# Performance work log

Hardware: AMD Instinct MI355X
Metric: run time of the kernel (lower is better)

Reference implementation:

```python
import jax, jax.numpy as jnp
import numpy as np

CHAR_SIZE, WORD_SIZE = 200, 100000
EC, EW, HID = 128, 300, 512
H2 = HID // 2
NW, TC = 1024, 16
POS, NER = 48, 16


def lstm_layer(x, Wih, Whh, b, reverse=False):
    """PyTorch-gate-order LSTM. x: [T, ..., D] -> [T, ..., H]."""
    H = Whh.shape[1]
    init = (jnp.zeros(x.shape[1:-1] + (H,), x.dtype),) * 2
    def step(carry, xt):
        h, c = carry
        z = xt @ Wih.T + h @ Whh.T + b
        i, f, g, o = jnp.split(z, 4, axis=-1)
        c = jax.nn.sigmoid(f) * c + jax.nn.sigmoid(i) * jnp.tanh(g)
        h = jax.nn.sigmoid(o) * jnp.tanh(c)
        return (h, c), h
    _, hs = jax.lax.scan(step, init, x, reverse=reverse)
    return hs


def bilstm(x, pf, pb):
    hf = lstm_layer(x, *pf)
    hb = lstm_layer(x, *pb, reverse=True)
    return jnp.concatenate([hf, hb], axis=-1)


def setup_inputs() -> dict:
    key = jax.random.key(0)
    ks = iter(jax.random.split(key, 40))
    def p(shape, s=0.05):
        return jax.random.normal(next(ks), shape, jnp.float32) * s
    d = {}
    d['char_emb'] = p((CHAR_SIZE, EC))
    d['word_emb'] = p((WORD_SIZE, EW))
    for pre, din in (('c', EC), ('w', EW + HID)):
        for sfx in ('f', 'b'):
            d[pre + 'Wih_' + sfx] = p((4 * H2, din))
            d[pre + 'Whh_' + sfx] = p((4 * H2, H2))
            d[pre + 'b_' + sfx] = p((4 * H2,))
    d['aW'] = p((HID, HID)); d['ab'] = p((HID,)); d['aw'] = p((HID,))
    d['hpW'] = p((POS, HID)); d['hpb'] = p((POS,))
    d['hnW'] = p((NER, HID)); d['hnb'] = p((NER,))
    d['word_seq'] = jax.random.randint(next(ks), (NW,), 0, WORD_SIZE)
    d['char_seq'] = jax.random.randint(next(ks), (NW, TC), 0, CHAR_SIZE)
    return d


def reference(char_emb, word_emb,
              cWih_f, cWhh_f, cb_f, cWih_b, cWhh_b, cb_b,
              wWih_f, wWhh_f, wb_f, wWih_b, wWhh_b, wb_b,
              aW, ab, aw, hpW, hpb, hnW, hnb,
              word_seq, char_seq):
    # --- per-word char BiLSTM, batched over all NW words (replaces Python loop) ---
    ce = char_emb[char_seq].transpose(1, 0, 2)              # [TC, NW, EC]
    enc = bilstm(ce, (cWih_f, cWhh_f, cb_f), (cWih_b, cWhh_b, cb_b))  # [TC, NW, HID]
    # --- 'self' attention pooling over char positions ---
    energy = jnp.tanh(enc @ aW.T + ab)                      # [TC, NW, HID]
    alpha = jax.nn.softmax(jnp.einsum('h,tnh->tn', aw, energy), axis=0)
    context = jnp.einsum('tn,tnh->nh', alpha, enc)          # [NW, HID]
    # --- word-level BiLSTM over the sentence (batch 1) ---
    x = jnp.concatenate([word_emb[word_seq], context], axis=1)  # [NW, EW+HID]
    out = bilstm(x, (wWih_f, wWhh_f, wb_f), (wWih_b, wWhh_b, wb_b))  # [NW, HID]
    pos = jax.nn.log_softmax(out @ hpW.T + hpb, axis=1)
    ner = jax.nn.log_softmax(out @ hnW.T + hnb, axis=1)
    return pos, ner
```

## Files before the change

kernel.cpp:

```cpp
#include <hip/hip_runtime.h>
#include <hip/hip_bf16.h>
#include <hip/hip_fp16.h>
#include <math.h>

#define NW 1024
#define TC 16
#define EC 128
#define EW 300
#define HID 512
#define H2 256
#define GATES 1024
#define KC (EC + H2)
#define KW (EW + HID)
#define NPOS 48
#define NNER 16

typedef _Float16 h2v __attribute__((ext_vector_type(2)));
union U32H { unsigned int u; h2v h; float f; };

__device__ __forceinline__ float sigf(float x) { return 1.f / (1.f + expf(-x)); }

__global__ __launch_bounds__(256)
void char_gate_gemm(int s,
    const float* __restrict__ char_emb, const int* __restrict__ char_seq,
    const float* __restrict__ Wih_f, const float* __restrict__ Whh_f,
    const float* __restrict__ Wih_b, const float* __restrict__ Whh_b,
    const float* __restrict__ hbuf,
    float* __restrict__ zbuf)
{
    const int d = blockIdx.z;
    const float* Wih = d ? Wih_b : Wih_f;
    const float* Whh = d ? Whh_b : Whh_f;
    const int t_time = d ? (TC - 1 - s) : s;
    const float* hprev = hbuf + (size_t)((s & 1) * 2 + d) * NW * H2;

    __shared__ float As[16][65];
    __shared__ float Bs[16][65];
    const int tid = threadIdx.x;
    const int tx = tid & 15, ty = tid >> 4;
    const int row0 = blockIdx.x * 64;
    const int col0 = blockIdx.y * 64;
    float acc[4][4] = {};
    for (int kb = 0; kb < KC; kb += 16) {
        #pragma unroll
        for (int q = 0; q < 4; ++q) {
            int idx = tid + q * 256;
            int mm = idx >> 4, kk = idx & 15;
            int k = kb + kk;
            int n = row0 + mm;
            float av;
            if (k < EC) {
                int ci = char_seq[n * TC + t_time];
                av = char_emb[(size_t)ci * EC + k];
            } else {
                av = (s == 0) ? 0.f : hprev[(size_t)n * H2 + (k - EC)];
            }
            As[kk][mm] = av;
            int g = col0 + mm;
            Bs[kk][mm] = (k < EC) ? Wih[(size_t)g * EC + k] : Whh[(size_t)g * H2 + (k - EC)];
        }
        __syncthreads();
        #pragma unroll
        for (int kk = 0; kk < 16; ++kk) {
            float a[4], b[4];
            #pragma unroll
            for (int i = 0; i < 4; ++i) a[i] = As[kk][ty * 4 + i];
            #pragma unroll
            for (int j = 0; j < 4; ++j) b[j] = Bs[kk][tx * 4 + j];
            #pragma unroll
            for (int i = 0; i < 4; ++i)
                #pragma unroll
                for (int j = 0; j < 4; ++j) acc[i][j] += a[i] * b[j];
        }
        __syncthreads();
    }
    float* zo = zbuf + (size_t)d * NW * GATES;
    #pragma unroll
    for (int i = 0; i < 4; ++i)
        #pragma unroll
        for (int j = 0; j < 4; ++j)
            zo[(size_t)(row0 + ty * 4 + i) * GATES + (col0 + tx * 4 + j)] = acc[i][j];
}

__global__ __launch_bounds__(256)
void char_pointwise(int s,
    const float* __restrict__ zbuf,
    const float* __restrict__ b_f, const float* __restrict__ b_b,
    float* __restrict__ hbuf,
    float* __restrict__ cbuf,
    float* __restrict__ enc)
{
    int id = blockIdx.x * blockDim.x + threadIdx.x;
    int d = id >> 18;
    int r = id & ((1 << 18) - 1);
    int n = r >> 8, j = r & (H2 - 1);
    const float* bias = d ? b_b : b_f;
    const float* z = zbuf + ((size_t)d * NW + n) * GATES;
    float zi = z[j]         + bias[j];
    float zf = z[H2 + j]    + bias[H2 + j];
    float zg = z[2*H2 + j]  + bias[2*H2 + j];
    float zo = z[3*H2 + j]  + bias[3*H2 + j];
    float c_old = (s == 0) ? 0.f : cbuf[(size_t)d * NW * H2 + r];
    float c = sigf(zf) * c_old + sigf(zi) * tanhf(zg);
    float h = sigf(zo) * tanhf(c);
    cbuf[(size_t)d * NW * H2 + r] = c;
    hbuf[(size_t)(((s + 1) & 1) * 2 + d) * NW * H2 + r] = h;
    int t_time = d ? (TC - 1 - s) : s;
    enc[((size_t)t_time * NW + n) * HID + d * H2 + j] = h;
}

__global__ __launch_bounds__(256)
void score_gemm(const float* __restrict__ enc, const float* __restrict__ aW,
                const float* __restrict__ ab, const float* __restrict__ aw,
                float* __restrict__ part)
{
    __shared__ float As[16][65];
    __shared__ float Bs[16][65];
    __shared__ float red[64][17];
    const int tid = threadIdx.x;
    const int tx = tid & 15, ty = tid >> 4;
    const int row0 = blockIdx.x * 64;
    const int col0 = blockIdx.y * 64;
    float acc[4][4] = {};
    for (int kb = 0; kb < HID; kb += 16) {
        #pragma unroll
        for (int q = 0; q < 4; ++q) {
            int idx = tid + q * 256;
            int mm = idx >> 4, kk = idx & 15;
            As[kk][mm] = enc[(size_t)(row0 + mm) * HID + kb + kk];
            Bs[kk][mm] = aW[(size_t)(col0 + mm) * HID + kb + kk];
        }
        __syncthreads();
        #pragma unroll
        for (int kk = 0; kk < 16; ++kk) {
            float a[4], b[4];
            #pragma unroll
            for (int i = 0; i < 4; ++i) a[i] = As[kk][ty * 4 + i];
            #pragma unroll
            for (int j = 0; j < 4; ++j) b[j] = Bs[kk][tx * 4 + j];
            #pragma unroll
            for (int i = 0; i < 4; ++i)
                #pragma unroll
                for (int j = 0; j < 4; ++j) acc[i][j] += a[i] * b[j];
        }
        __syncthreads();
    }
    #pragma unroll
    for (int i = 0; i < 4; ++i) {
        float rs = 0.f;
        #pragma unroll
        for (int j = 0; j < 4; ++j) {
            int col = col0 + tx * 4 + j;
            rs += tanhf(acc[i][j] + ab[col]) * aw[col];
        }
        red[ty * 4 + i][tx] = rs;
    }
    __syncthreads();
    if (tid < 64) {
        float v = 0.f;
        #pragma unroll
        for (int x = 0; x < 16; ++x) v += red[tid][x];
        part[(size_t)(row0 + tid) * 8 + blockIdx.y] = v;
    }
}

__global__ void alpha_softmax(const float* __restrict__ part, float* __restrict__ al)
{
    int n = blockIdx.x * blockDim.x + threadIdx.x;
    float sc[TC];
    #pragma unroll
    for (int t = 0; t < TC; ++t) {
        float v = 0.f;
        #pragma unroll
        for (int q = 0; q < 8; ++q) v += part[(size_t)(t * NW + n) * 8 + q];
        sc[t] = v;
    }
    float m = -1e30f;
    #pragma unroll
    for (int t = 0; t < TC; ++t) m = fmaxf(m, sc[t]);
    float ssum = 0.f;
    #pragma unroll
    for (int t = 0; t < TC; ++t) { sc[t] = expf(sc[t] - m); ssum += sc[t]; }
    float inv = 1.f / ssum;
    #pragma unroll
    for (int t = 0; t < TC; ++t) al[t * NW + n] = sc[t] * inv;
}

__global__ void context_kernel(const float* __restrict__ al, const float* __restrict__ enc,
                               float* __restrict__ ctx)
{
    int id = blockIdx.x * blockDim.x + threadIdx.x;
    int n = id >> 9, h = id & (HID - 1);
    float v = 0.f;
    #pragma unroll
    for (int t = 0; t < TC; ++t)
        v += al[t * NW + n] * enc[((size_t)t * NW + n) * HID + h];
    ctx[id] = v;
}

__global__ __launch_bounds__(256)
void word_proj_gemm(const float* __restrict__ word_emb, const int* __restrict__ word_seq,
                    const float* __restrict__ ctx,
                    const float* __restrict__ Wih_f, const float* __restrict__ b_fp,
                    const float* __restrict__ Wih_b, const float* __restrict__ b_bp,
                    float* __restrict__ Gw)
{
    const int d = blockIdx.z;
    const float* W = d ? Wih_b : Wih_f;
    const float* bias = d ? b_bp : b_fp;
    __shared__ float As[16][65];
    __shared__ float Bs[16][65];
    const int tid = threadIdx.x;
    const int tx = tid & 15, ty = tid >> 4;
    const int row0 = blockIdx.x * 64;
    const int col0 = blockIdx.y * 64;
    float acc[4][4] = {};
    for (int kb = 0; kb < KW; kb += 16) {
        #pragma unroll
        for (int q = 0; q < 4; ++q) {
            int idx = tid + q * 256;
            int mm = idx >> 4, kk = idx & 15;
            int k = kb + kk;
            int n = row0 + mm;
            float av = 0.f, bv = 0.f;
            if (k < KW) {
                if (k < EW) av = word_emb[(size_t)word_seq[n] * EW + k];
                else        av = ctx[(size_t)n * HID + (k - EW)];
                bv = W[(size_t)(col0 + mm) * KW + k];
            }
            As[kk][mm] = av;
            Bs[kk][mm] = bv;
        }
        __syncthreads();
        #pragma unroll
        for (int kk = 0; kk < 16; ++kk) {
            float a[4], b[4];
            #pragma unroll
            for (int i = 0; i < 4; ++i) a[i] = As[kk][ty * 4 + i];
            #pragma unroll
            for (int j = 0; j < 4; ++j) b[j] = Bs[kk][tx * 4 + j];
            #pragma unroll
            for (int i = 0; i < 4; ++i)
                #pragma unroll
                for (int j = 0; j < 4; ++j) acc[i][j] += a[i] * b[j];
        }
        __syncthreads();
    }
    float* zo = Gw + (size_t)d * NW * GATES;
    #pragma unroll
    for (int i = 0; i < 4; ++i)
        #pragma unroll
        for (int j = 0; j < 4; ++j) {
            int g = col0 + tx * 4 + j;
            zo[(size_t)(row0 + ty * 4 + i) * GATES + g] = acc[i][j] + bias[g];
        }
}

__global__ __launch_bounds__(512, 2)
void word_lstm_dir(const float* __restrict__ Whh_fw, const float* __restrict__ Whh_bw,
                   const float* __restrict__ Gw,
                   float* __restrict__ wout)
{
    extern __shared__ float smem[];
    unsigned int* lw = (unsigned int*)smem;
    float* zs = smem + 64 * 512;
    unsigned int* hpk = (unsigned int*)(zs + GATES);

    const int d = blockIdx.x;
    const int tid = threadIdx.x;
    const float* Whh = d ? Whh_bw : Whh_fw;
    const float* G = Gw + (size_t)d * NW * GATES;

    const float* r0 = Whh + (size_t)tid * H2;
    const float* r1 = Whh + (size_t)(tid + 512) * H2;
    h2v wv0[96], wv1[96];
    #pragma unroll
    for (int p = 0; p < 96; ++p) {
        h2v w; w.x = (_Float16)r0[2*p]; w.y = (_Float16)r0[2*p+1]; wv0[p] = w;
        h2v v; v.x = (_Float16)r1[2*p]; v.y = (_Float16)r1[2*p+1]; wv1[p] = v;
    }
    #pragma unroll
    for (int p = 96; p < 128; ++p) {
        U32H a; a.h.x = (_Float16)r0[2*p]; a.h.y = (_Float16)r0[2*p+1];
        lw[(p - 96) * 512 + tid] = a.u;
        U32H b; b.h.x = (_Float16)r1[2*p]; b.h.y = (_Float16)r1[2*p+1];
        lw[(p - 96 + 32) * 512 + tid] = b.u;
    }
    if (tid < 128) hpk[tid] = 0u;
    float c0 = 0.f, c1 = 0.f;
    __syncthreads();

    const int woff = d * H2;
    for (int t = 0; t < NW; ++t) {
        const int tt = d ? (NW - 1 - t) : t;
        float g0 = G[(size_t)tt * GATES + tid];
        float g1 = G[(size_t)tt * GATES + 512 + tid];
        float acc0 = 0.f, acc1 = 0.f;
        const uint4* hp4 = (const uint4*)hpk;
        #pragma unroll
        for (int q = 0; q < 32; ++q) {
            uint4 hh = hp4[q];
            #pragma unroll
            for (int r = 0; r < 4; ++r) {
                const int p = q * 4 + r;
                U32H hu; hu.u = (&hh.x)[r];
                h2v w0, w1;
                if (p < 96) { w0 = wv0[p]; w1 = wv1[p]; }
                else {
                    U32H a; a.u = lw[(p - 96) * 512 + tid]; w0 = a.h;
                    U32H b; b.u = lw[(p - 96 + 32) * 512 + tid]; w1 = b.h;
                }
                acc0 = __builtin_amdgcn_fdot2(hu.h, w0, acc0, false);
                acc1 = __builtin_amdgcn_fdot2(hu.h, w1, acc1, false);
            }
        }
        zs[tid] = acc0 + g0;
        zs[512 + tid] = acc1 + g1;
        __syncthreads();
        if (tid < 128) {
            const int u0 = 2 * tid, u1 = u0 + 1;
            float zi0 = zs[u0],       zi1 = zs[u1];
            float zf0 = zs[256 + u0], zf1 = zs[256 + u1];
            float zg0 = zs[512 + u0], zg1 = zs[512 + u1];
            float zo0 = zs[768 + u0], zo1 = zs[768 + u1];
            c0 = sigf(zf0) * c0 + sigf(zi0) * tanhf(zg0);
            float h0 = sigf(zo0) * tanhf(c0);
            c1 = sigf(zf1) * c1 + sigf(zi1) * tanhf(zg1);
            float h1 = sigf(zo1) * tanhf(c1);
            U32H hp; hp.h.x = (_Float16)h0; hp.h.y = (_Float16)h1;
            hpk[tid] = hp.u;
            float2 hv; hv.x = h0; hv.y = h1;
            *(float2*)&wout[(size_t)tt * HID + woff + u0] = hv;
        }
        __syncthreads();
    }
}

__global__ __launch_bounds__(64)
void heads_kernel(const float* __restrict__ wout,
                  const float* __restrict__ hpW, const float* __restrict__ hpb,
                  const float* __restrict__ hnW, const float* __restrict__ hnb,
                  float* __restrict__ out)
{
    const int n = blockIdx.x;
    const int tid = threadIdx.x;
    __shared__ float v[HID];
    #pragma unroll
    for (int q = 0; q < 8; ++q) v[tid + q * 64] = wout[(size_t)n * HID + tid + q * 64];
    __syncthreads();
    float sc = 0.f;
    if (tid < NPOS) {
        for (int k = 0; k < HID; ++k) sc += v[k] * hpW[(size_t)tid * HID + k];
        sc += hpb[tid];
    } else {
        int cc = tid - NPOS;
        for (int k = 0; k < HID; ++k) sc += v[k] * hnW[(size_t)cc * HID + k];
        sc += hnb[cc];
    }
    __shared__ float ssc[64];
    __shared__ float lsep, lsen;
    ssc[tid] = sc;
    __syncthreads();
    if (tid == 0) {
        float m = -1e30f;
        for (int i = 0; i < NPOS; ++i) m = fmaxf(m, ssc[i]);
        float su = 0.f;
        for (int i = 0; i < NPOS; ++i) su += expf(ssc[i] - m);
        lsep = m + logf(su);
    }
    if (tid == 32) {
        float m = -1e30f;
        for (int i = NPOS; i < 64; ++i) m = fmaxf(m, ssc[i]);
        float su = 0.f;
        for (int i = NPOS; i < 64; ++i) su += expf(ssc[i] - m);
        lsen = m + logf(su);
    }
    __syncthreads();
    if (tid < NPOS) out[(size_t)n * NPOS + tid] = sc - lsep;
    else            out[(size_t)NW * NPOS + (size_t)n * NNER + (tid - NPOS)] = sc - lsen;
}

extern "C" void kernel_launch(void* const* d_in, const int* in_sizes, int n_in,
                              void* d_out, int out_size, void* d_ws, size_t ws_size,
                              hipStream_t stream) {
    const float* char_emb = (const float*)d_in[0];
    const float* word_emb = (const float*)d_in[1];
    const float* cWih_f   = (const float*)d_in[2];
    const float* cWhh_f   = (const float*)d_in[3];
    const float* cb_f     = (const float*)d_in[4];
    const float* cWih_b   = (const float*)d_in[5];
    const float* cWhh_b   = (const float*)d_in[6];
    const float* cb_b     = (const float*)d_in[7];
    const float* wWih_f   = (const float*)d_in[8];
    const float* wWhh_f   = (const float*)d_in[9];
    const float* wb_f     = (const float*)d_in[10];
    const float* wWih_b   = (const float*)d_in[11];
    const float* wWhh_b   = (const float*)d_in[12];
    const float* wb_b     = (const float*)d_in[13];
    const float* aW       = (const float*)d_in[14];
    const float* ab       = (const float*)d_in[15];
    const float* aw       = (const float*)d_in[16];
    const float* hpW      = (const float*)d_in[17];
    const float* hpb      = (const float*)d_in[18];
    const float* hnW      = (const float*)d_in[19];
    const float* hnb      = (const float*)d_in[20];
    const int*   word_seq = (const int*)d_in[21];
    const int*   char_seq = (const int*)d_in[22];
    float* out = (float*)d_out;
    float* ws  = (float*)d_ws;

    const size_t OFF_ENC  = 0;
    const size_t OFF_Z    = OFF_ENC  + (size_t)TC * NW * HID;
    const size_t OFF_CH   = OFF_Z    + (size_t)2 * NW * GATES;
    const size_t OFF_CC   = OFF_CH   + (size_t)4 * NW * H2;
    const size_t OFF_CTX  = OFF_CC   + (size_t)2 * NW * H2;
    const size_t OFF_WOUT = OFF_CTX  + (size_t)NW * HID;
    const size_t OFF_PART = OFF_WOUT + (size_t)NW * HID;
    const size_t OFF_AL   = OFF_PART + (size_t)TC * NW * 8;

    dim3 gchar(NW / 64, GATES / 64, 2);
    for (int s = 0; s < TC; ++s) {
        char_gate_gemm<<<gchar, 256, 0, stream>>>(s, char_emb, char_seq,
            cWih_f, cWhh_f, cWih_b, cWhh_b, ws + OFF_CH, ws + OFF_Z);
        char_pointwise<<<(2 * NW * H2) / 256, 256, 0, stream>>>(s, ws + OFF_Z,
            cb_f, cb_b, ws + OFF_CH, ws + OFF_CC, ws + OFF_ENC);
    }

    score_gemm<<<dim3(TC * NW / 64, HID / 64), 256, 0, stream>>>(
        ws + OFF_ENC, aW, ab, aw, ws + OFF_PART);
    alpha_softmax<<<NW / 256, 256, 0, stream>>>(ws + OFF_PART, ws + OFF_AL);
    context_kernel<<<(NW * HID) / 256, 256, 0, stream>>>(ws + OFF_AL, ws + OFF_ENC, ws + OFF_CTX);

    word_proj_gemm<<<dim3(NW / 64, GATES / 64, 2), 256, 0, stream>>>(
        word_emb, word_seq, ws + OFF_CTX, wWih_f, wb_f, wWih_b, wb_b, ws + OFF_Z);

    const int lds_bytes = (64 * 512 + GATES + 128) * 4;
    hipFuncSetAttribute((const void*)word_lstm_dir,
                        hipFuncAttributeMaxDynamicSharedMemorySize, lds_bytes);
    word_lstm_dir<<<2, 512, lds_bytes, stream>>>(wWhh_f, wWhh_b, ws + OFF_Z, ws + OFF_WOUT);

    heads_kernel<<<NW, 64, 0, stream>>>(ws + OFF_WOUT, hpW, hpb, hnW, hnb, out);
}
```

Before: 4.237 ms.

## Use one thread per gate row in word LSTM, prefetch next gate input

```diff
diff --git a/kernel.cpp b/kernel.cpp
--- a/kernel.cpp
+++ b/kernel.cpp
@@ -256,14 +256,14 @@
         }
 }
 
-__global__ __launch_bounds__(512, 2)
+__global__ __launch_bounds__(1024)
 void word_lstm_dir(const float* __restrict__ Whh_fw, const float* __restrict__ Whh_bw,
                    const float* __restrict__ Gw,
                    float* __restrict__ wout)
 {
     extern __shared__ float smem[];
     unsigned int* lw = (unsigned int*)smem;
-    float* zs = smem + 64 * 512;
+    float* zs = smem + 32 * 1024;
     unsigned int* hpk = (unsigned int*)(zs + GATES);
 
     const int d = blockIdx.x;
@@ -272,66 +272,68 @@
     const float* G = Gw + (size_t)d * NW * GATES;
 
     const float* r0 = Whh + (size_t)tid * H2;
-    const float* r1 = Whh + (size_t)(tid + 512) * H2;
-    h2v wv0[96], wv1[96];
+    h2v wv[96];
     #pragma unroll
     for (int p = 0; p < 96; ++p) {
-        h2v w; w.x = (_Float16)r0[2*p]; w.y = (_Float16)r0[2*p+1]; wv0[p] = w;
-        h2v v; v.x = (_Float16)r1[2*p]; v.y = (_Float16)r1[2*p+1]; wv1[p] = v;
-    }
-    #pragma unroll
-    for (int p = 96; p < 128; ++p) {
+        h2v w; w.x = (_Float16)r0[2*p]; w.y = (_Float16)r0[2*p+1]; wv[p] = w;
+    }
+    #pragma unroll
+    for (int s = 0; s < 32; ++s) {
+        int p = 96 + s;
         U32H a; a.h.x = (_Float16)r0[2*p]; a.h.y = (_Float16)r0[2*p+1];
-        lw[(p - 96) * 512 + tid] = a.u;
-        U32H b; b.h.x = (_Float16)r1[2*p]; b.h.y = (_Float16)r1[2*p+1];
-        lw[(p - 96 + 32) * 512 + tid] = b.u;
+        lw[(s >> 1) * 2048 + tid * 2 + (s & 1)] = a.u;
     }
     if (tid < 128) hpk[tid] = 0u;
-    float c0 = 0.f, c1 = 0.f;
+    float c = 0.f;
     __syncthreads();
 
     const int woff = d * H2;
+    float g = G[(size_t)(d ? (NW - 1) : 0) * GATES + tid];
     for (int t = 0; t < NW; ++t) {
         const int tt = d ? (NW - 1 - t) : t;
-        float g0 = G[(size_t)tt * GATES + tid];
-        float g1 = G[(size_t)tt * GATES + 512 + tid];
-        float acc0 = 0.f, acc1 = 0.f;
+        float gn = 0.f;
+        if (t + 1 < NW) {
+            const int tn = d ? (NW - 2 - t) : (t + 1);
+            gn = G[(size_t)tn * GATES + tid];
+        }
+        float a0 = 0.f, a1 = 0.f, a2 = 0.f, a3 = 0.f;
         const uint4* hp4 = (const uint4*)hpk;
         #pragma unroll
-        for (int q = 0; q < 32; ++q) {
+        for (int q = 0; q < 24; ++q) {
             uint4 hh = hp4[q];
-            #pragma unroll
-            for (int r = 0; r < 4; ++r) {
-                const int p = q * 4 + r;
-                U32H hu; hu.u = (&hh.x)[r];
-                h2v w0, w1;
-                if (p < 96) { w0 = wv0[p]; w1 = wv1[p]; }
-                else {
-                    U32H a; a.u = lw[(p - 96) * 512 + tid]; w0 = a.h;
-                    U32H b; b.u = lw[(p - 96 + 32) * 512 + tid]; w1 = b.h;
-                }
-                acc0 = __builtin_amdgcn_fdot2(hu.h, w0, acc0, false);
-                acc1 = __builtin_amdgcn_fdot2(hu.h, w1, acc1, false);
-            }
-        }
-        zs[tid] = acc0 + g0;
-        zs[512 + tid] = acc1 + g1;
-        __syncthreads();
-        if (tid < 128) {
-            const int u0 = 2 * tid, u1 = u0 + 1;
-            float zi0 = zs[u0],       zi1 = zs[u1];
-            float zf0 = zs[256 + u0], zf1 = zs[256 + u1];
-            float zg0 = zs[512 + u0], zg1 = zs[512 + u1];
-            float zo0 = zs[768 + u0], zo1 = zs[768 + u1];
-            c0 = sigf(zf0) * c0 + sigf(zi0) * tanhf(zg0);
-            float h0 = sigf(zo0) * tanhf(c0);
-            c1 = sigf(zf1) * c1 + sigf(zi1) * tanhf(zg1);
-            float h1 = sigf(zo1) * tanhf(c1);
-            U32H hp; hp.h.x = (_Float16)h0; hp.h.y = (_Float16)h1;
-            hpk[tid] = hp.u;
-            float2 hv; hv.x = h0; hv.y = h1;
-            *(float2*)&wout[(size_t)tt * HID + woff + u0] = hv;
-        }
+            U32H h0, h1, h2, h3;
+            h0.u = hh.x; h1.u = hh.y; h2.u = hh.z; h3.u = hh.w;
+            a0 = __builtin_amdgcn_fdot2(h0.h, wv[4*q],     a0, false);
+            a1 = __builtin_amdgcn_fdot2(h1.h, wv[4*q + 1], a1, false);
+            a2 = __builtin_amdgcn_fdot2(h2.h, wv[4*q + 2], a2, false);
+            a3 = __builtin_amdgcn_fdot2(h3.h, wv[4*q + 3], a3, false);
+        }
+        #pragma unroll
+        for (int q = 24; q < 32; ++q) {
+            uint4 hh = hp4[q];
+            const int r = (q - 24) * 2;
+            uint2 wa = *(const uint2*)&lw[r * 2048 + tid * 2];
+            uint2 wb = *(const uint2*)&lw[(r + 1) * 2048 + tid * 2];
+            U32H h0, h1, h2, h3;
+            h0.u = hh.x; h1.u = hh.y; h2.u = hh.z; h3.u = hh.w;
+            U32H w0; w0.u = wa.x; U32H w1; w1.u = wa.y;
+            U32H w2; w2.u = wb.x; U32H w3; w3.u = wb.y;
+            a0 = __builtin_amdgcn_fdot2(h0.h, w0.h, a0, false);
+            a1 = __builtin_amdgcn_fdot2(h1.h, w1.h, a1, false);
+            a2 = __builtin_amdgcn_fdot2(h2.h, w2.h, a2, false);
+            a3 = __builtin_amdgcn_fdot2(h3.h, w3.h, a3, false);
+        }
+        zs[tid] = (a0 + a1) + (a2 + a3) + g;
+        __syncthreads();
+        if (tid < H2) {
+            float zi = zs[tid],        zf = zs[H2 + tid];
+            float zg = zs[2*H2 + tid], zo = zs[3*H2 + tid];
+            c = sigf(zf) * c + sigf(zi) * tanhf(zg);
+            float h = sigf(zo) * tanhf(c);
+            ((_Float16*)hpk)[tid] = (_Float16)h;
+            wout[(size_t)tt * HID + woff + tid] = h;
+        }
+        g = gn;
         __syncthreads();
     }
 }
@@ -434,10 +436,10 @@
     word_proj_gemm<<<dim3(NW / 64, GATES / 64, 2), 256, 0, stream>>>(
         word_emb, word_seq, ws + OFF_CTX, wWih_f, wb_f, wWih_b, wb_b, ws + OFF_Z);
 
-    const int lds_bytes = (64 * 512 + GATES + 128) * 4;
+    const int lds_bytes = (32 * 1024 + GATES + 128) * 4;
     hipFuncSetAttribute((const void*)word_lstm_dir,
                         hipFuncAttributeMaxDynamicSharedMemorySize, lds_bytes);
-    word_lstm_dir<<<2, 512, lds_bytes, stream>>>(wWhh_f, wWhh_b, ws + OFF_Z, ws + OFF_WOUT);
+    word_lstm_dir<<<2, 1024, lds_bytes, stream>>>(wWhh_f, wWhh_b, ws + OFF_Z, ws + OFF_WOUT);
 
     heads_kernel<<<NW, 64, 0, stream>>>(ws + OFF_WOUT, hpW, hpb, hnW, hnb, out);
 }
```

Result: faster. 3.733 ms (-11.9%).
